# Kernel optimization log

Measured on AMD Instinct MI355X. Metric: run time of the kernel, lower is better.

The kernel has to match this reference:

```python
import jax, jax.numpy as jnp
import numpy as np

D_MODEL = 1024
NUM_HEADS = 16
D_K = D_MODEL // NUM_HEADS


def setup_inputs() -> dict:
    key = jax.random.key(0)
    ks = jax.random.split(key, 12)
    B, S = 4, 2048
    scale = 1.0 / np.sqrt(D_MODEL)
    inp = {
        "query": jax.random.normal(ks[0], (B, S, D_MODEL), dtype=jnp.float32),
        "key": jax.random.normal(ks[1], (B, S, D_MODEL), dtype=jnp.float32),
        "value": jax.random.normal(ks[2], (B, S, D_MODEL), dtype=jnp.float32),
        "Wq": jax.random.normal(ks[3], (D_MODEL, D_MODEL), dtype=jnp.float32) * scale,
        "bq": jnp.zeros((D_MODEL,), dtype=jnp.float32),
        "Wk": jax.random.normal(ks[4], (D_MODEL, D_MODEL), dtype=jnp.float32) * scale,
        "bk": jnp.zeros((D_MODEL,), dtype=jnp.float32),
        "Wv": jax.random.normal(ks[5], (D_MODEL, D_MODEL), dtype=jnp.float32) * scale,
        "bv": jnp.zeros((D_MODEL,), dtype=jnp.float32),
        "Wo": jax.random.normal(ks[6], (D_MODEL, D_MODEL), dtype=jnp.float32) * scale,
        "bo": jnp.zeros((D_MODEL,), dtype=jnp.float32),
    }
    return inp


def reference(query, key, value, Wq, bq, Wk, bk, Wv, bv, Wo, bo):
    B, S, _ = query.shape
    # project and split heads: [B, S, D] -> [B, H, S, d_k]
    def split_heads(x):
        return x.reshape(B, -1, NUM_HEADS, D_K).transpose(0, 2, 1, 3)

    q = split_heads(query @ Wq + bq)
    k = split_heads(key @ Wk + bk)
    v = split_heads(value @ Wv + bv)

    # scores: [B, H, Sq, Sk]
    scores = jnp.einsum("bhqd,bhkd->bhqk", q, k) / jnp.sqrt(jnp.float32(D_K))
    p_attn = jax.nn.softmax(scores, axis=-1)
    out = jnp.einsum("bhqk,bhkd->bhqd", p_attn, v)  # [B, H, Sq, d_k]

    out = out.transpose(0, 2, 1, 3).reshape(B, -1, NUM_HEADS * D_K)
    return out @ Wo + bo
```

## Files before the change

### kernel.cpp

```cpp
#include <hip/hip_runtime.h>
#include <hip/hip_bf16.h>

#define D_MODEL 1024
#define SEQ     2048
#define BATCH   4
#define HEADS   16
#define DKK     64
#define MTOT    (BATCH*SEQ)

typedef __attribute__((ext_vector_type(8)))  __bf16 bf16x8;
typedef __attribute__((ext_vector_type(4)))  float  f32x4;
typedef __attribute__((ext_vector_type(16))) float  f32x16;
typedef unsigned short u16;
typedef __attribute__((address_space(1))) const unsigned GU;
typedef __attribute__((address_space(3))) unsigned LU;

__device__ __forceinline__ u16 f2bf(float f) {
    unsigned u = __builtin_bit_cast(unsigned, f);
    u += 0x7FFFu + ((u >> 16) & 1u);
    return (u16)(u >> 16);
}

__device__ __forceinline__ unsigned pk2(float a, float b) {
    u16 x = __builtin_bit_cast(u16, (__bf16)a);
    u16 y = __builtin_bit_cast(u16, (__bf16)b);
    return (unsigned)x | ((unsigned)y << 16);
}

__device__ __forceinline__ float exp2_hw(float x) {
    return __builtin_amdgcn_exp2f(x);
}

__global__ void f2b3_kernel(const float* __restrict__ q, const float* __restrict__ k,
                            const float* __restrict__ v,
                            u16* __restrict__ oq, u16* __restrict__ ok, u16* __restrict__ ov,
                            int n4) {
    const float* in = (blockIdx.y == 0) ? q : (blockIdx.y == 1) ? k : v;
    u16* out = (blockIdx.y == 0) ? oq : (blockIdx.y == 1) ? ok : ov;
    int stride = gridDim.x * blockDim.x;
    for (int i = blockIdx.x * blockDim.x + threadIdx.x; i < n4; i += stride) {
        float4 x = reinterpret_cast<const float4*>(in)[i];
        ushort4 o;
        o.x = f2bf(x.x); o.y = f2bf(x.y); o.z = f2bf(x.z); o.w = f2bf(x.w);
        reinterpret_cast<ushort4*>(out)[i] = o;
    }
}

__global__ void wtrans4_kernel(const float* __restrict__ W0, const float* __restrict__ W1,
                               const float* __restrict__ W2, const float* __restrict__ W3,
                               u16* __restrict__ T0, u16* __restrict__ T1,
                               u16* __restrict__ T2, u16* __restrict__ T3) {
    const float* W = (blockIdx.z == 0) ? W0 : (blockIdx.z == 1) ? W1 : (blockIdx.z == 2) ? W2 : W3;
    u16* Wt = (blockIdx.z == 0) ? T0 : (blockIdx.z == 1) ? T1 : (blockIdx.z == 2) ? T2 : T3;
    __shared__ float t[32][33];
    int bx = blockIdx.x * 32, by = blockIdx.y * 32;
    int x = threadIdx.x, y0 = threadIdx.y;
    for (int y = y0; y < 32; y += 8)
        t[y][x] = W[(size_t)(by + y) * D_MODEL + bx + x];
    __syncthreads();
    for (int y = y0; y < 32; y += 8)
        Wt[(size_t)(bx + y) * D_MODEL + by + x] = f2bf(t[x][y]);
}

__global__ __launch_bounds__(256) void gemm_pipe(
        const u16* __restrict__ A0, const u16* __restrict__ A1, const u16* __restrict__ A2,
        const u16* __restrict__ B0, const u16* __restrict__ B1, const u16* __restrict__ B2,
        const float* __restrict__ bi0, const float* __restrict__ bi1, const float* __restrict__ bi2,
        u16* __restrict__ o0, u16* __restrict__ o1, u16* __restrict__ o2,
        float* __restrict__ outf, int mode, float scale0)
{
    __shared__ __align__(16) char smem[3][16384];

    const int z = blockIdx.z;
    const u16* A  = (z == 0) ? A0 : (z == 1) ? A1 : A2;
    const u16* Bt = (z == 0) ? B0 : (z == 1) ? B1 : B2;
    const float* bias = (z == 0) ? bi0 : (z == 1) ? bi1 : bi2;
    u16* outb = (z == 0) ? o0 : (z == 1) ? o1 : o2;
    const float scale = (z == 0) ? scale0 : 1.0f;

    const int tid = threadIdx.x;
    const int m0 = blockIdx.y * 128, n0 = blockIdx.x * 128;
    const int w = tid >> 6, lane = tid & 63;
    const int l15 = lane & 15, lg = lane >> 4;
    const int wr = w >> 1, wc = w & 1;

    f32x4 acc[4][4];
#pragma unroll
    for (int i = 0; i < 4; i++)
#pragma unroll
        for (int j = 0; j < 4; j++) acc[i][j] = (f32x4){0.f, 0.f, 0.f, 0.f};

    auto stage = [&](int buf, int k0) {
        u16* Al = (u16*)(smem[buf]);
        u16* Bl = (u16*)(smem[buf] + 8192);
#pragma unroll
        for (int c = tid; c < 512; c += 256) {
            int row = c >> 2, ch = c & 3;
            __builtin_amdgcn_global_load_lds(
                (GU*)(A + (size_t)(m0 + row) * D_MODEL + k0 + ch * 8),
                (LU*)(Al + c * 8), 16, 0, 0);
            __builtin_amdgcn_global_load_lds(
                (GU*)(Bt + (size_t)(n0 + row) * D_MODEL + k0 + ch * 8),
                (LU*)(Bl + c * 8), 16, 0, 0);
        }
    };

    auto compute = [&](int buf) {
        const u16* Al = (const u16*)(smem[buf]);
        const u16* Bl = (const u16*)(smem[buf] + 8192);
        bf16x8 af[4], bfr[4];
#pragma unroll
        for (int m = 0; m < 4; m++)
            af[m] = *reinterpret_cast<const bf16x8*>(&Al[(wr * 64 + m * 16 + l15) * 32 + lg * 8]);
#pragma unroll
        for (int n = 0; n < 4; n++)
            bfr[n] = *reinterpret_cast<const bf16x8*>(&Bl[(wc * 64 + n * 16 + l15) * 32 + lg * 8]);
        __builtin_amdgcn_s_setprio(1);
#pragma unroll
        for (int m = 0; m < 4; m++)
#pragma unroll
            for (int n = 0; n < 4; n++)
                acc[m][n] = __builtin_amdgcn_mfma_f32_16x16x32_bf16(af[m], bfr[n], acc[m][n], 0, 0, 0);
        __builtin_amdgcn_s_setprio(0);
    };

    stage(0, 0);
    stage(1, 32);
    for (int t = 0; t < 32; ++t) {
        if (t < 31) asm volatile("s_waitcnt vmcnt(4)" ::: "memory");
        else        asm volatile("s_waitcnt vmcnt(0)" ::: "memory");
        __builtin_amdgcn_s_barrier();
        __builtin_amdgcn_sched_barrier(0);
        if (t + 2 < 32) stage((t + 2) % 3, (t + 2) * 32);
        compute(t % 3);
    }

#pragma unroll
    for (int n = 0; n < 4; n++) {
        int col = n0 + wc * 64 + n * 16 + l15;
        float bv = bias[col];
        int h = col >> 6, d = col & 63;
#pragma unroll
        for (int m = 0; m < 4; m++) {
            int rowb = m0 + wr * 64 + m * 16 + lg * 4;
            if (mode == 0) {
                int b = rowb >> 11, s0r = rowb & (SEQ - 1);
                if (z == 2) {
                    ushort4 pk;
                    pk.x = f2bf(acc[m][n][0] + bv);
                    pk.y = f2bf(acc[m][n][1] + bv);
                    pk.z = f2bf(acc[m][n][2] + bv);
                    pk.w = f2bf(acc[m][n][3] + bv);
                    *reinterpret_cast<ushort4*>(
                        &outb[(((size_t)b * HEADS + h) * DKK + d) * SEQ + s0r]) = pk;
                } else {
#pragma unroll
                    for (int r = 0; r < 4; r++)
                        outb[(((size_t)b * HEADS + h) * SEQ + s0r + r) * DKK + d] =
                            f2bf((acc[m][n][r] + bv) * scale);
                }
            } else {
#pragma unroll
                for (int r = 0; r < 4; r++)
                    outf[(size_t)(rowb + r) * D_MODEL + col] = acc[m][n][r] + bv;
            }
        }
    }
}

__global__ __launch_bounds__(512, 2) void attn9_kernel(
        const u16* __restrict__ Qh, const u16* __restrict__ Kh,
        const u16* __restrict__ VT, u16* __restrict__ ctx)
{
    __shared__ __align__(16) char smem[3][16384];

    const int i = blockIdx.x;
    const int xcd = i & 7, j = i >> 3;
    const int bh = xcd + 8 * (j & 7);
    const int bx = j >> 3;
    const int b = bh >> 4, h = bh & 15;
    const int tid = threadIdx.x, w = tid >> 6, lane = tid & 63;
    const int l31 = lane & 31, hi = lane >> 5;
    const int q0 = bx * 256 + w * 32;

    const u16* Qp = Qh + ((size_t)bh * SEQ + q0 + l31) * DKK + 8 * hi;
    bf16x8 qf[4];
#pragma unroll
    for (int c = 0; c < 4; c++)
        qf[c] = *reinterpret_cast<const bf16x8*>(Qp + 16 * c);

    const char* Kbyte = (const char*)(Kh + (size_t)bh * SEQ * DKK);
    const char* Vbyte = (const char*)(VT + (size_t)bh * DKK * SEQ);

    f32x16 zv;
#pragma unroll
    for (int z = 0; z < 16; z++) zv[z] = 0.f;
    f32x16 oacc0 = zv, oacc1 = zv;
    float lsum = 0.f;

    const int kr = tid >> 3, kc = tid & 7;
    const int ksw = (kc ^ (kr & 7)) * 16;
    const int krp = (kr & 51) | ((kr & 4) << 1) | ((kr & 8) >> 1);

    auto stage = [&](int buf, int kt) {
        char* Kb = smem[buf];
        char* Vb = smem[buf] + 8192;
        __builtin_amdgcn_global_load_lds((GU*)(Kbyte + (size_t)(kt + krp) * 128 + ksw),
                                         (LU*)(Kb + tid * 16), 16, 0, 0);
        __builtin_amdgcn_global_load_lds((GU*)(Vbyte + (size_t)kr * (SEQ * 2) + kt * 2 + ksw),
                                         (LU*)(Vb + tid * 16), 16, 0, 0);
    };

    auto compute = [&](int buf) {
        const char* Kb = smem[buf];
        const char* Vb = smem[buf] + 8192;
        const int xr = (l31 & 7);

        bf16x8 kf[8];
#pragma unroll
        for (int c = 0; c < 4; c++) {
            int sl = ((2 * c + hi) ^ xr) * 16;
            kf[c]     = *reinterpret_cast<const bf16x8*>(Kb + l31 * 128 + sl);
            kf[c + 4] = *reinterpret_cast<const bf16x8*>(Kb + (l31 + 32) * 128 + sl);
        }

        __builtin_amdgcn_s_setprio(1);
        f32x16 s0 = __builtin_amdgcn_mfma_f32_32x32x16_bf16(kf[0], qf[0], zv, 0, 0, 0);
        f32x16 s1 = __builtin_amdgcn_mfma_f32_32x32x16_bf16(kf[4], qf[0], zv, 0, 0, 0);
#pragma unroll
        for (int c = 1; c < 4; c++) {
            s0 = __builtin_amdgcn_mfma_f32_32x32x16_bf16(kf[c],     qf[c], s0, 0, 0, 0);
            s1 = __builtin_amdgcn_mfma_f32_32x32x16_bf16(kf[c + 4], qf[c], s1, 0, 0, 0);
        }
        __builtin_amdgcn_s_setprio(0);

#pragma unroll
        for (int i2 = 0; i2 < 16; i2++) { s0[i2] = exp2_hw(s0[i2]); s1[i2] = exp2_hw(s1[i2]); }
        float a0 = (s0[0] + s0[1]) + (s0[2] + s0[3]);
        float a1 = (s0[4] + s0[5]) + (s0[6] + s0[7]);
        float a2 = (s0[8] + s0[9]) + (s0[10] + s0[11]);
        float a3 = (s0[12] + s0[13]) + (s0[14] + s0[15]);
        float b0 = (s1[0] + s1[1]) + (s1[2] + s1[3]);
        float b1 = (s1[4] + s1[5]) + (s1[6] + s1[7]);
        float b2 = (s1[8] + s1[9]) + (s1[10] + s1[11]);
        float b3 = (s1[12] + s1[13]) + (s1[14] + s1[15]);
        lsum += ((a0 + a1) + (a2 + a3)) + ((b0 + b1) + (b2 + b3));

#pragma unroll
        for (int t = 0; t < 4; t++) {
            const int o = 8 * (t & 1);
            union { unsigned u[4]; bf16x8 v; } pu;
            if (t < 2) {
                pu.u[0] = pk2(s0[o+0], s0[o+1]);
                pu.u[1] = pk2(s0[o+2], s0[o+3]);
                pu.u[2] = pk2(s0[o+4], s0[o+5]);
                pu.u[3] = pk2(s0[o+6], s0[o+7]);
            } else {
                pu.u[0] = pk2(s1[o+0], s1[o+1]);
                pu.u[1] = pk2(s1[o+2], s1[o+3]);
                pu.u[2] = pk2(s1[o+4], s1[o+5]);
                pu.u[3] = pk2(s1[o+6], s1[o+7]);
            }
            bf16x8 pf = pu.v;

            int sl = ((2 * t + hi) ^ xr) * 16;
            bf16x8 vf0 = *reinterpret_cast<const bf16x8*>(Vb + l31 * 128 + sl);
            bf16x8 vf1 = *reinterpret_cast<const bf16x8*>(Vb + (l31 + 32) * 128 + sl);
            __builtin_amdgcn_s_setprio(1);
            oacc0 = __builtin_amdgcn_mfma_f32_32x32x16_bf16(vf0, pf, oacc0, 0, 0, 0);
            oacc1 = __builtin_amdgcn_mfma_f32_32x32x16_bf16(vf1, pf, oacc1, 0, 0, 0);
            __builtin_amdgcn_s_setprio(0);
        }
    };

    stage(0, 0);
    stage(1, 64);
    for (int t = 0; t < 32; ++t) {
        if (t < 31) asm volatile("s_waitcnt vmcnt(2)" ::: "memory");
        else        asm volatile("s_waitcnt vmcnt(0)" ::: "memory");
        __builtin_amdgcn_s_barrier();
        __builtin_amdgcn_sched_barrier(0);
        if (t + 2 < 32) stage((t + 2) % 3, (t + 2) * 64);
        compute(t % 3);
    }
    __syncthreads();

    lsum += __shfl_xor(lsum, 32, 64);
    float inv = 1.0f / lsum;

    typedef u16 OtArr[32][72];
    OtArr* Ot = reinterpret_cast<OtArr*>(smem);
#pragma unroll
    for (int r = 0; r < 16; r++) {
        int d0 = (r & 3) + 8 * (r >> 2) + 4 * hi;
        Ot[w][l31][d0]      = f2bf(oacc0[r] * inv);
        Ot[w][l31][d0 + 32] = f2bf(oacc1[r] * inv);
    }
    __syncthreads();
#pragma unroll
    for (int it = 0; it < 4; it++) {
        int r = (lane >> 3) + 8 * it, ch = lane & 7;
        bf16x8 v = *reinterpret_cast<const bf16x8*>(&Ot[w][r][ch * 8]);
        *reinterpret_cast<bf16x8*>(ctx + ((size_t)b * SEQ + q0 + r) * D_MODEL + h * DKK + ch * 8) = v;
    }
}

extern "C" void kernel_launch(void* const* d_in, const int* in_sizes, int n_in,
                              void* d_out, int out_size, void* d_ws, size_t ws_size,
                              hipStream_t stream)
{
    (void)in_sizes; (void)n_in; (void)out_size; (void)ws_size;

    const float* query = (const float*)d_in[0];
    const float* key   = (const float*)d_in[1];
    const float* value = (const float*)d_in[2];
    const float* Wq    = (const float*)d_in[3];
    const float* bq    = (const float*)d_in[4];
    const float* Wk    = (const float*)d_in[5];
    const float* bk    = (const float*)d_in[6];
    const float* Wv    = (const float*)d_in[7];
    const float* bv    = (const float*)d_in[8];
    const float* Wo    = (const float*)d_in[9];
    const float* bo    = (const float*)d_in[10];
    float* out = (float*)d_out;

    char* ws = (char*)d_ws;
    const size_t MB = 1024ull * 1024ull;
    u16* Xq  = (u16*)(ws);
    u16* Xk  = (u16*)(ws + 16 * MB);
    u16* Xv  = (u16*)(ws + 32 * MB);
    u16* Wtq = (u16*)(ws + 48 * MB);
    u16* Wtk = (u16*)(ws + 50 * MB);
    u16* Wtv = (u16*)(ws + 52 * MB);
    u16* Wto = (u16*)(ws + 54 * MB);
    u16* Qhp = (u16*)(ws + 56 * MB);
    u16* Khp = (u16*)(ws + 72 * MB);
    u16* VT  = (u16*)(ws + 88 * MB);
    u16* ctx = (u16*)(ws + 104 * MB);

    int nX4 = MTOT * D_MODEL / 4;
    f2b3_kernel<<<dim3(1024, 3), 256, 0, stream>>>(query, key, value, Xq, Xk, Xv, nX4);

    dim3 wg(32, 32, 4), wb(32, 8);
    wtrans4_kernel<<<wg, wb, 0, stream>>>(Wq, Wk, Wv, Wo, Wtq, Wtk, Wtv, Wto);

    dim3 g3(D_MODEL / 128, MTOT / 128, 3);
    gemm_pipe<<<g3, 256, 0, stream>>>(Xq, Xk, Xv, Wtq, Wtk, Wtv, bq, bk, bv,
                                      Qhp, Khp, VT, nullptr, 0, 0.125f * 1.44269504f);

    attn9_kernel<<<512, 512, 0, stream>>>(Qhp, Khp, VT, ctx);

    dim3 g1(D_MODEL / 128, MTOT / 128, 1);
    gemm_pipe<<<g1, 256, 0, stream>>>(ctx, ctx, ctx, Wto, Wto, Wto, bo, bo, bo,
                                      nullptr, nullptr, nullptr, out, 1, 1.0f);
}
```

Before: 221.6 us.

## Remap GEMM blocks per XCD and stage V-transpose epilogue through LDS

Result: faster. 207.0 us (-6.6%).

```diff
diff --git a/kernel.cpp b/kernel.cpp
--- a/kernel.cpp
+++ b/kernel.cpp
@@ -71,7 +71,15 @@
 {
     __shared__ __align__(16) char smem[3][16384];
 
-    const int z = blockIdx.z;
+    const int lin = blockIdx.x;
+    const int xcd = lin & 7, slot = lin >> 3;
+    const int cpx = gridDim.x >> 3;
+    const int work = xcd * cpx + slot;
+    const int xb = work & 7;
+    const int yz = work >> 3;
+    const int z = yz >> 6, yb = yz & 63;
+    const int m0 = yb * 128, n0 = xb * 128;
+
     const u16* A  = (z == 0) ? A0 : (z == 1) ? A1 : A2;
     const u16* Bt = (z == 0) ? B0 : (z == 1) ? B1 : B2;
     const float* bias = (z == 0) ? bi0 : (z == 1) ? bi1 : bi2;
@@ -79,7 +87,6 @@
     const float scale = (z == 0) ? scale0 : 1.0f;
 
     const int tid = threadIdx.x;
-    const int m0 = blockIdx.y * 128, n0 = blockIdx.x * 128;
     const int w = tid >> 6, lane = tid & 63;
     const int l15 = lane & 15, lg = lane >> 4;
     const int wr = w >> 1, wc = w & 1;
@@ -135,6 +142,37 @@
         compute(t % 3);
     }
 
+    if (mode == 0 && z == 2) {
+        __syncthreads();
+        typedef u16 TRow[136];
+        TRow* T = reinterpret_cast<TRow*>(smem);
+#pragma unroll
+        for (int n = 0; n < 4; n++) {
+            int colL = wc * 64 + n * 16 + l15;
+            float bv = bias[n0 + colL];
+#pragma unroll
+            for (int m = 0; m < 4; m++) {
+                int rowL = wr * 64 + m * 16 + lg * 4;
+#pragma unroll
+                for (int r = 0; r < 4; r++)
+                    T[colL][rowL + r] = f2bf(acc[m][n][r] + bv);
+            }
+        }
+        __syncthreads();
+        {
+            int col = tid >> 1, half = tid & 1;
+            int colG = n0 + col;
+            int h = colG >> 6, d = colG & 63;
+            int b = m0 >> 11, s0r = (m0 & (SEQ - 1)) + half * 64;
+            u16* dst = outb + (((size_t)b * HEADS + h) * DKK + d) * SEQ + s0r;
+            const u16* src = &T[col][half * 64];
+#pragma unroll
+            for (int c = 0; c < 8; c++)
+                *reinterpret_cast<bf16x8*>(dst + c * 8) =
+                    *reinterpret_cast<const bf16x8*>(src + c * 8);
+        }
+        return;
+    }
 #pragma unroll
     for (int n = 0; n < 4; n++) {
         int col = n0 + wc * 64 + n * 16 + l15;
@@ -145,20 +183,10 @@
             int rowb = m0 + wr * 64 + m * 16 + lg * 4;
             if (mode == 0) {
                 int b = rowb >> 11, s0r = rowb & (SEQ - 1);
-                if (z == 2) {
-                    ushort4 pk;
-                    pk.x = f2bf(acc[m][n][0] + bv);
-                    pk.y = f2bf(acc[m][n][1] + bv);
-                    pk.z = f2bf(acc[m][n][2] + bv);
-                    pk.w = f2bf(acc[m][n][3] + bv);
-                    *reinterpret_cast<ushort4*>(
-                        &outb[(((size_t)b * HEADS + h) * DKK + d) * SEQ + s0r]) = pk;
-                } else {
-#pragma unroll
-                    for (int r = 0; r < 4; r++)
-                        outb[(((size_t)b * HEADS + h) * SEQ + s0r + r) * DKK + d] =
-                            f2bf((acc[m][n][r] + bv) * scale);
-                }
+#pragma unroll
+                for (int r = 0; r < 4; r++)
+                    outb[(((size_t)b * HEADS + h) * SEQ + s0r + r) * DKK + d] =
+                        f2bf((acc[m][n][r] + bv) * scale);
             } else {
 #pragma unroll
                 for (int r = 0; r < 4; r++)
@@ -344,13 +372,11 @@
     dim3 wg(32, 32, 4), wb(32, 8);
     wtrans4_kernel<<<wg, wb, 0, stream>>>(Wq, Wk, Wv, Wo, Wtq, Wtk, Wtv, Wto);
 
-    dim3 g3(D_MODEL / 128, MTOT / 128, 3);
-    gemm_pipe<<<g3, 256, 0, stream>>>(Xq, Xk, Xv, Wtq, Wtk, Wtv, bq, bk, bv,
-                                      Qhp, Khp, VT, nullptr, 0, 0.125f * 1.44269504f);
+    gemm_pipe<<<1536, 256, 0, stream>>>(Xq, Xk, Xv, Wtq, Wtk, Wtv, bq, bk, bv,
+                                        Qhp, Khp, VT, nullptr, 0, 0.125f * 1.44269504f);
 
     attn9_kernel<<<512, 512, 0, stream>>>(Qhp, Khp, VT, ctx);
 
-    dim3 g1(D_MODEL / 128, MTOT / 128, 1);
-    gemm_pipe<<<g1, 256, 0, stream>>>(ctx, ctx, ctx, Wto, Wto, Wto, bo, bo, bo,
-                                      nullptr, nullptr, nullptr, out, 1, 1.0f);
-}
+    gemm_pipe<<<512, 256, 0, stream>>>(ctx, ctx, ctx, Wto, Wto, Wto, bo, bo, bo,
+                                       nullptr, nullptr, nullptr, out, 1, 1.0f);
+}
```
